# Kernel tuning notes

Hardware: AMD Instinct MI355X
Metric: run time of the kernel (lower is better)

Reference implementation:

```python
import jax, jax.numpy as jnp
import numpy as np

MAX_DISP = 192

def _conv(x, w, b=None, stride=1, pad=0):
    y = jax.lax.conv_general_dilated(x, w, (stride, stride), [(pad, pad), (pad, pad)],
                                     dimension_numbers=('NCHW', 'OIHW', 'NCHW'))
    return y if b is None else y + b[None, :, None, None]

def _inorm(x):  # InstanceNorm2d, affine=False
    m = x.mean((2, 3), keepdims=True)
    v = x.var((2, 3), keepdims=True)
    return (x - m) * jax.lax.rsqrt(v + 1e-5)

def _bnorm(x):  # BatchNorm2d at init (gamma=1, beta=0), batch stats
    m = x.mean((0, 2, 3), keepdims=True)
    v = x.var((0, 2, 3), keepdims=True)
    return (x - m) * jax.lax.rsqrt(v + 1e-5)

def _encoder(x, w1, b1, w2, b2, w3, b3, norm):
    # simplified BasicEncoder: two stride-2 convs -> 1/4 resolution, then 1x1 proj
    x = jax.nn.relu(norm(_conv(x, w1, b1, 2, 3)))
    x = jax.nn.relu(norm(_conv(x, w2, b2, 2, 1)))
    return _conv(x, w3, b3, 1, 0)

def _forward(image1, image2, fnet_w1, fnet_b1, fnet_w2, fnet_b2, fnet_w3, fnet_b3,
             cnet_w1, cnet_b1, cnet_w2, cnet_b2, cnet_w3, cnet_b3,
             bform_a, bform_b, bform_cd_w, bform_cd_b,
             gru_wz, gru_bz, gru_wr, gru_br, gru_wq, gru_bq,
             disp_w1, disp_b1, disp_w2, disp_b2):
    i1 = 2.0 * (image1 / 255.0) - 1.0
    i2 = 2.0 * (image2 / 255.0) - 1.0
    fmap1 = _encoder(i1, fnet_w1, fnet_b1, fnet_w2, fnet_b2, fnet_w3, fnet_b3, _inorm)
    fmap2 = _encoder(i2, fnet_w1, fnet_b1, fnet_w2, fnet_b2, fnet_w3, fnet_b3, _inorm)
    hidden = jnp.tanh(_encoder(i1, cnet_w1, cnet_b1, cnet_w2, cnet_b2, cnet_w3, cnet_b3, _bnorm))
    Wf = fmap1.shape[3]
    for d in range(MAX_DISP // 4):  # 48 sequential width-sweep steps, shrinking overlap
        f1 = fmap1[:, :, :, d:]
        f2 = fmap2[:, :, :, :Wf - d] if d > 0 else fmap2
        # BilinearForm: a(x) + b(y) + cd(x*y), all 1x1 convs
        feat = _conv(f1, bform_a) + _conv(f2, bform_b) + _conv(f1 * f2, bform_cd_w, bform_cd_b)
        h = hidden[:, :, :, d:]
        # gru_input = cat(h, feat); ConvGRU cats hidden again -> [h, h, feat] = 96 ch
        hx = jnp.concatenate([h, h, feat], axis=1)
        z = jax.nn.sigmoid(_conv(hx, gru_wz, gru_bz, 1, 1))
        r = jax.nn.sigmoid(_conv(hx, gru_wr, gru_br, 1, 1))
        q = jnp.tanh(_conv(jnp.concatenate([r * h, h, feat], axis=1), gru_wq, gru_bq, 1, 1))
        h = (1.0 - z) * h + z * q
        hidden = hidden.at[:, :, :, d:].set(h)  # in-place scatter back
    # DisparityHead: conv3x3 -> relu -> conv3x3, negated
    return -_conv(jax.nn.relu(_conv(hidden, disp_w1, disp_b1, 1, 1)), disp_w2, disp_b2, 1, 1)

def setup_inputs():
    key = jax.random.key(0)
    ks = jax.random.split(key, 16)
    B, H, W, D = 1, 384, 640, 32
    def n(k, shape, scale=0.05):
        return (jax.random.normal(k, shape) * scale).astype(jnp.float32)
    z = lambda c: jnp.zeros((c,), jnp.float32)
    return {
        'image1': jax.random.uniform(ks[0], (B, 3, H, W), jnp.float32) * 255.0,
        'image2': jax.random.uniform(ks[1], (B, 3, H, W), jnp.float32) * 255.0,
        'fnet_w1': n(ks[2], (D, 3, 7, 7)), 'fnet_b1': z(D),
        'fnet_w2': n(ks[3], (D, D, 3, 3)), 'fnet_b2': z(D),
        'fnet_w3': n(ks[4], (D, D, 1, 1)), 'fnet_b3': z(D),
        'cnet_w1': n(ks[5], (D, 3, 7, 7)), 'cnet_b1': z(D),
        'cnet_w2': n(ks[6], (D, D, 3, 3)), 'cnet_b2': z(D),
        'cnet_w3': n(ks[7], (D, D, 1, 1)), 'cnet_b3': z(D),
        'bform_a': n(ks[8], (D, D, 1, 1)), 'bform_b': n(ks[9], (D, D, 1, 1)),
        'bform_cd_w': n(ks[10], (D, D, 1, 1)), 'bform_cd_b': z(D),
        'gru_wz': n(ks[11], (D, 3 * D, 3, 3)), 'gru_bz': z(D),
        'gru_wr': n(ks[12], (D, 3 * D, 3, 3)), 'gru_br': z(D),
        'gru_wq': n(ks[13], (D, 3 * D, 3, 3)), 'gru_bq': z(D),
        'disp_w1': n(ks[14], (64, D, 3, 3)), 'disp_b1': z(64),
        'disp_w2': n(ks[15], (1, 64, 3, 3)), 'disp_b2': z(1),
    }

def reference(image1, image2, fnet_w1, fnet_b1, fnet_w2, fnet_b2, fnet_w3, fnet_b3,
              cnet_w1, cnet_b1, cnet_w2, cnet_b2, cnet_w3, cnet_b3,
              bform_a, bform_b, bform_cd_w, bform_cd_b,
              gru_wz, gru_bz, gru_wr, gru_br, gru_wq, gru_bq,
              disp_w1, disp_b1, disp_w2, disp_b2):
    return _forward(image1, image2, fnet_w1, fnet_b1, fnet_w2, fnet_b2, fnet_w3, fnet_b3,
                    cnet_w1, cnet_b1, cnet_w2, cnet_b2, cnet_w3, cnet_b3,
                    bform_a, bform_b, bform_cd_w, bform_cd_b,
                    gru_wz, gru_bz, gru_wr, gru_br, gru_wq, gru_bq,
                    disp_w1, disp_b1, disp_w2, disp_b2)
```

## Files before the change

kernel.cpp:

```cpp
#include <hip/hip_runtime.h>
#include <math.h>

#define H0 384
#define W0 640
#define H1 192
#define W1 320
#define H2 96
#define W2 160
#define NP1 (H1*W1)
#define NP2 (H2*W2)
#define ND  48
#define NBLK2 (NP2/256)
#define CHW ((size_t)32*NP2)
#define PW 162
#define PH 98
#define PSL (PH*PW)
#define PCHW ((size_t)32*PSL)

typedef float v2f __attribute__((ext_vector_type(2)));


__global__ void zero_buf_kernel(float* __restrict__ p, size_t n) {
    size_t i = (size_t)blockIdx.x*256 + threadIdx.x;
    size_t stride = (size_t)gridDim.x*256;
    for (; i < n; i += stride) p[i] = 0.f;
}

__device__ __forceinline__ void twr_dev(const float* __restrict__ in, float* __restrict__ out,
                                        int idx, int CI, int K, int CO) {
    int co = idx % CO;
    int t  = idx / CO;
    int k  = t % K;
    int ci = t / K;
    out[idx] = in[(co*CI + ci)*K + k];
}

__global__ void prep_all(const float* __restrict__ fnet_w1, const float* __restrict__ cnet_w1,
                         const float* __restrict__ fnet_w2, const float* __restrict__ cnet_w2,
                         const float* __restrict__ fnet_w3, const float* __restrict__ cnet_w3,
                         const float* __restrict__ bform_a, const float* __restrict__ bform_b,
                         const float* __restrict__ bform_cd_w, const float* __restrict__ disp_w1,
                         const float* __restrict__ gru_wz, const float* __restrict__ gru_wr,
                         const float* __restrict__ gru_wq,
                         float* __restrict__ we1f, float* __restrict__ we1c,
                         float* __restrict__ we2f, float* __restrict__ we2c,
                         float* __restrict__ w3f, float* __restrict__ w3c,
                         float* __restrict__ wat, float* __restrict__ wbt,
                         float* __restrict__ wct, float* __restrict__ wd1t,
                         float4* __restrict__ wzrpk, float2* __restrict__ wqpk,
                         float* __restrict__ stats) {
    int i = blockIdx.x*256 + threadIdx.x;
    if (i < 4704) { twr_dev(fnet_w1, we1f, i, 3, 49, 32); return; }
    i -= 4704;
    if (i < 4704) { twr_dev(cnet_w1, we1c, i, 3, 49, 32); return; }
    i -= 4704;
    if (i < 9216) { twr_dev(fnet_w2, we2f, i, 32, 9, 32); return; }
    i -= 9216;
    if (i < 9216) { twr_dev(cnet_w2, we2c, i, 32, 9, 32); return; }
    i -= 9216;
    if (i < 1024) { twr_dev(fnet_w3, w3f, i, 32, 1, 32); return; }
    i -= 1024;
    if (i < 1024) { twr_dev(cnet_w3, w3c, i, 32, 1, 32); return; }
    i -= 1024;
    if (i < 1024) { twr_dev(bform_a, wat, i, 32, 1, 32); return; }
    i -= 1024;
    if (i < 1024) { twr_dev(bform_b, wbt, i, 32, 1, 32); return; }
    i -= 1024;
    if (i < 1024) { twr_dev(bform_cd_w, wct, i, 32, 1, 32); return; }
    i -= 1024;
    if (i < 18432) { twr_dev(disp_w1, wd1t, i, 32, 9, 64); return; }
    i -= 18432;
    if (i < 9216) {
        int k  = i % 9;
        int ci = (i/9) % 64;
        int cg = i / (9*64);
        int co0 = cg*2, co1 = co0 + 1;
        float z0, z1, r0, r1;
        if (ci < 32) {
            z0 = gru_wz[(co0*96 + ci)*9 + k] + gru_wz[(co0*96 + ci + 32)*9 + k];
            z1 = gru_wz[(co1*96 + ci)*9 + k] + gru_wz[(co1*96 + ci + 32)*9 + k];
            r0 = gru_wr[(co0*96 + ci)*9 + k] + gru_wr[(co0*96 + ci + 32)*9 + k];
            r1 = gru_wr[(co1*96 + ci)*9 + k] + gru_wr[(co1*96 + ci + 32)*9 + k];
        } else {
            z0 = gru_wz[(co0*96 + ci + 32)*9 + k];
            z1 = gru_wz[(co1*96 + ci + 32)*9 + k];
            r0 = gru_wr[(co0*96 + ci + 32)*9 + k];
            r1 = gru_wr[(co1*96 + ci + 32)*9 + k];
        }
        wzrpk[i] = make_float4(z0, z1, r0, r1);
        return;
    }
    i -= 9216;
    if (i < 13824) {
        int k  = i % 9;
        int ci = (i/9) % 96;
        int cg = i / (9*96);
        wqpk[i] = make_float2(gru_wq[((cg*2)*96 + ci)*9 + k], gru_wq[((cg*2+1)*96 + ci)*9 + k]);
        return;
    }
    i -= 13824;
    if (i < 384) stats[i] = 0.f;
}

__global__ void pad_init_kernel(const float* __restrict__ hidden, float* __restrict__ hwork) {
    int idx = blockIdx.x*256 + threadIdx.x;
    if (idx >= 32*PSL) return;
    int c = idx / PSL;
    int r = idx % PSL;
    int py = r / PW, px = r % PW;
    int y = py - 1, x = px - 1;
    float v = 0.f;
    if ((unsigned)y < (unsigned)H2 && (unsigned)x < (unsigned)W2)
        v = hidden[c*NP2 + y*W2 + x];
    hwork[idx] = v;
}


__global__ __launch_bounds__(256, 4)
void conv7s2_dual(const float* __restrict__ img,
                  const float* __restrict__ wtf, const float* __restrict__ wtc,
                  const float* __restrict__ bf, const float* __restrict__ bc,
                  float* __restrict__ outf, float* __restrict__ outc) {
    int co8 = blockIdx.y*8;
    int sp = blockIdx.x*256 + threadIdx.x;
    int oy = sp / W1, ox = sp % W1;
    float af[8], ac[8];
    #pragma unroll
    for (int j = 0; j < 8; ++j) { af[j] = bf[co8+j]; ac[j] = bc[co8+j]; }
    for (int ci = 0; ci < 3; ++ci) {
        for (int ky = 0; ky < 7; ++ky) {
            int iy = 2*oy - 3 + ky;
            if ((unsigned)iy >= (unsigned)H0) continue;
            const float* row  = img + ci*(H0*W0) + iy*W0;
            int wbase = (ci*49 + ky*7)*32 + co8;
            #pragma unroll
            for (int kx = 0; kx < 7; ++kx) {
                int ix = 2*ox - 3 + kx;
                if ((unsigned)ix >= (unsigned)W0) continue;
                float v = row[ix]*(2.0f/255.0f) - 1.0f;
                const float4* wpf = (const float4*)(wtf + wbase + kx*32);
                const float4* wpc = (const float4*)(wtc + wbase + kx*32);
                float4 f0 = wpf[0], f1 = wpf[1];
                float4 c0 = wpc[0], c1 = wpc[1];
                af[0] += v*f0.x; af[1] += v*f0.y; af[2] += v*f0.z; af[3] += v*f0.w;
                af[4] += v*f1.x; af[5] += v*f1.y; af[6] += v*f1.z; af[7] += v*f1.w;
                ac[0] += v*c0.x; ac[1] += v*c0.y; ac[2] += v*c0.z; ac[3] += v*c0.w;
                ac[4] += v*c1.x; ac[5] += v*c1.y; ac[6] += v*c1.z; ac[7] += v*c1.w;
            }
        }
    }
    #pragma unroll
    for (int j = 0; j < 8; ++j) {
        outf[(co8+j)*NP1 + sp] = af[j];
        outc[(co8+j)*NP1 + sp] = ac[j];
    }
}

__global__ void conv7s2_v3(const float* __restrict__ img, const float* __restrict__ wt,
                           const float* __restrict__ b, float* __restrict__ out) {
    int cg = blockIdx.y;
    int co16 = cg*16;
    int sp = blockIdx.x*256 + threadIdx.x;
    int oy = sp / W1, ox = sp % W1;
    float acc[16];
    #pragma unroll
    for (int j = 0; j < 16; ++j) acc[j] = b[co16+j];
    for (int ci = 0; ci < 3; ++ci) {
        for (int ky = 0; ky < 7; ++ky) {
            int iy = 2*oy - 3 + ky;
            if ((unsigned)iy >= (unsigned)H0) continue;
            const float* row  = img + ci*(H0*W0) + iy*W0;
            const float* wrow = wt + (ci*49 + ky*7)*32 + co16;
            #pragma unroll
            for (int kx = 0; kx < 7; ++kx) {
                int ix = 2*ox - 3 + kx;
                if ((unsigned)ix >= (unsigned)W0) continue;
                float v = row[ix]*(2.0f/255.0f) - 1.0f;
                const float4* wp = (const float4*)(wrow + kx*32);
                #pragma unroll
                for (int j4 = 0; j4 < 4; ++j4) {
                    float4 w4 = wp[j4];
                    acc[4*j4+0] += v*w4.x; acc[4*j4+1] += v*w4.y;
                    acc[4*j4+2] += v*w4.z; acc[4*j4+3] += v*w4.w;
                }
            }
        }
    }
    #pragma unroll
    for (int j = 0; j < 16; ++j) out[(co16+j)*NP1 + sp] = acc[j];
}

__global__ void stats_partial_kernel(const float* __restrict__ x, int N, float* __restrict__ st) {
    int c = blockIdx.x >> 3, sl = blockIdx.x & 7;
    int chunk = N >> 3;
    const float4* p = (const float4*)(x + (size_t)c*N + (size_t)sl*chunk);
    int n4 = chunk >> 2;
    float s = 0.f, s2 = 0.f;
    for (int i = threadIdx.x; i < n4; i += 256) {
        float4 v = p[i];
        s  += v.x + v.y + v.z + v.w;
        s2 += v.x*v.x + v.y*v.y + v.z*v.z + v.w*v.w;
    }
    __shared__ float sh1[256], sh2[256];
    sh1[threadIdx.x] = s; sh2[threadIdx.x] = s2;
    __syncthreads();
    for (int o = 128; o > 0; o >>= 1) {
        if (threadIdx.x < o) { sh1[threadIdx.x] += sh1[threadIdx.x+o]; sh2[threadIdx.x] += sh2[threadIdx.x+o]; }
        __syncthreads();
    }
    if (threadIdx.x == 0) { atomicAdd(&st[2*c], sh1[0]); atomicAdd(&st[2*c+1], sh2[0]); }
}

__global__ void conv3s2_fused(const float* __restrict__ in, const float* __restrict__ st,
                              const float* __restrict__ wt, const float* __restrict__ b,
                              float* __restrict__ out) {
    int cg = blockIdx.x / NBLK2;
    int sp = (blockIdx.x % NBLK2)*256 + threadIdx.x;
    int co8 = cg*8;
    int oy = sp / W2, ox = sp % W2;
    float acc[8];
    #pragma unroll
    for (int j = 0; j < 8; ++j) acc[j] = b[co8+j];
    for (int ci = 0; ci < 32; ++ci) {
        float m    = st[2*ci] * (1.0f/NP1);
        float var  = st[2*ci+1] * (1.0f/NP1) - m*m;
        float rstd = rsqrtf(var + 1e-5f);
        const float* ip  = in + ci*NP1;
        const float* wci = wt + ci*9*32 + co8;
        #pragma unroll
        for (int ky = 0; ky < 3; ++ky) {
            int iy = 2*oy - 1 + ky;
            if ((unsigned)iy >= (unsigned)H1) continue;
            const float* row = ip + iy*W1;
            #pragma unroll
            for (int kx = 0; kx < 3; ++kx) {
                int ix = 2*ox - 1 + kx;
                if ((unsigned)ix >= (unsigned)W1) continue;
                float t = fmaxf((row[ix] - m)*rstd, 0.f);
                const float4* wp = (const float4*)(wci + (ky*3+kx)*32);
                float4 w0 = wp[0], w1 = wp[1];
                acc[0] += t*w0.x; acc[1] += t*w0.y; acc[2] += t*w0.z; acc[3] += t*w0.w;
                acc[4] += t*w1.x; acc[5] += t*w1.y; acc[6] += t*w1.z; acc[7] += t*w1.w;
            }
        }
    }
    #pragma unroll
    for (int j = 0; j < 8; ++j) out[(co8+j)*NP2 + sp] = acc[j];
}

__global__ void conv1x1_fused(const float* __restrict__ in, const float* __restrict__ st,
                              const float* __restrict__ wt, const float* __restrict__ b,
                              float* __restrict__ out, int mode) {
    int cg = blockIdx.x / NBLK2;
    int sp = (blockIdx.x % NBLK2)*256 + threadIdx.x;
    int co8 = cg*8;
    float acc[8];
    #pragma unroll
    for (int j = 0; j < 8; ++j) acc[j] = b[co8+j];
    for (int ci = 0; ci < 32; ++ci) {
        float m    = st[2*ci] * (1.0f/NP2);
        float var  = st[2*ci+1] * (1.0f/NP2) - m*m;
        float rstd = rsqrtf(var + 1e-5f);
        float t = fmaxf((in[ci*NP2 + sp] - m)*rstd, 0.f);
        const float4* wp = (const float4*)(wt + ci*32 + co8);
        float4 w0 = wp[0], w1 = wp[1];
        acc[0] += t*w0.x; acc[1] += t*w0.y; acc[2] += t*w0.z; acc[3] += t*w0.w;
        acc[4] += t*w1.x; acc[5] += t*w1.y; acc[6] += t*w1.z; acc[7] += t*w1.w;
    }
    #pragma unroll
    for (int j = 0; j < 8; ++j) {
        float a = acc[j];
        if (mode) a = tanhf(a);
        out[(co8+j)*NP2 + sp] = a;
    }
}


__global__ void feat0_pad_kernel(const float* __restrict__ fmap1, const float* __restrict__ fmap2,
                                 const float* __restrict__ wat, const float* __restrict__ wbt,
                                 const float* __restrict__ wct, const float* __restrict__ bc,
                                 float* __restrict__ featA) {
    int cg  = blockIdx.x / NBLK2;
    int sp  = (blockIdx.x % NBLK2)*256 + threadIdx.x;
    int y = sp / W2;
    int gx = sp % W2;
    int co8 = cg*8;
    float acc[8];
    #pragma unroll
    for (int j = 0; j < 8; ++j) acc[j] = bc[co8+j];
    for (int ci = 0; ci < 32; ++ci) {
        float f1 = fmap1[ci*NP2 + sp];
        float f2 = fmap2[ci*NP2 + sp];
        float f12 = f1*f2;
        const float4* ap = (const float4*)(wat + ci*32 + co8);
        const float4* bp = (const float4*)(wbt + ci*32 + co8);
        const float4* cp = (const float4*)(wct + ci*32 + co8);
        float4 a0 = ap[0], a1 = ap[1];
        float4 b0 = bp[0], b1 = bp[1];
        float4 c0 = cp[0], c1 = cp[1];
        acc[0] += f1*a0.x + f2*b0.x + f12*c0.x;
        acc[1] += f1*a0.y + f2*b0.y + f12*c0.y;
        acc[2] += f1*a0.z + f2*b0.z + f12*c0.z;
        acc[3] += f1*a0.w + f2*b0.w + f12*c0.w;
        acc[4] += f1*a1.x + f2*b1.x + f12*c1.x;
        acc[5] += f1*a1.y + f2*b1.y + f12*c1.y;
        acc[6] += f1*a1.z + f2*b1.z + f12*c1.z;
        acc[7] += f1*a1.w + f2*b1.w + f12*c1.w;
    }
    float* dst = featA + (size_t)(y+1)*PW + (gx+1);
    #pragma unroll
    for (int j = 0; j < 8; ++j) dst[(size_t)(co8+j)*PSL] = acc[j];
}


__global__ __launch_bounds__(256, 4)
void zrf_v6(const float* __restrict__ hworkA, const float* __restrict__ featA,
            const float* __restrict__ fmap1, const float* __restrict__ fmap2,
            const float4* __restrict__ wzrpk,
            const float* __restrict__ wat, const float* __restrict__ wbt,
            const float* __restrict__ wct, const float* __restrict__ bfc,
            const float* __restrict__ bz, const float* __restrict__ br,
            float* __restrict__ zbuf, float* __restrict__ rhpad,
            float* __restrict__ featB, int d, int Wd) {
    __shared__ v2f lwz[64*9], lwr[64*9];
    __shared__ v2f lfa[32], lfb[32], lfc[32];
    int cg  = blockIdx.y;
    int co0 = cg*2;
    {
        const float4* wsrc = wzrpk + (size_t)cg*576;
        for (int i = threadIdx.x; i < 576; i += 256) {
            float4 w = wsrc[i];
            lwz[i] = (v2f){w.x, w.y};
            lwr[i] = (v2f){w.z, w.w};
        }
        if (threadIdx.x < 32) {
            int ci = threadIdx.x;
            lfa[ci] = (v2f){wat[ci*32+co0], wat[ci*32+co0+1]};
            lfb[ci] = (v2f){wbt[ci*32+co0], wbt[ci*32+co0+1]};
            lfc[ci] = (v2f){wct[ci*32+co0], wct[ci*32+co0+1]};
        }
    }
    __syncthreads();
    int sp2 = blockIdx.x*256 + threadIdx.x;
    if (sp2 >= 48*Wd) return;
    int rp = sp2 / Wd;
    int lx = sp2 - rp*Wd;
    int y0 = rp*2;
    int gx = d + lx;
    size_t poff = (size_t)(y0+1)*PW + (gx+1);

    if (lx == 0) {
        #pragma unroll
        for (int j = 0; j < 2; ++j) {
            rhpad[(size_t)(co0+j)*PSL + poff - 1]      = 0.f;
            rhpad[(size_t)(co0+j)*PSL + poff + PW - 1] = 0.f;
        }
    }

    int dn = d + 1;
    if (dn < ND) {
        if (lx == 0) {
            #pragma unroll
            for (int j = 0; j < 2; ++j) {
                featB[(size_t)(co0+j)*PSL + poff]      = 0.f;
                featB[(size_t)(co0+j)*PSL + poff + PW] = 0.f;
            }
        } else {
            v2f f0 = (v2f){bfc[co0], bfc[co0+1]};
            v2f f1 = f0;
            int base1 = y0*W2 + gx;
            #pragma unroll 2
            for (int ci = 0; ci < 32; ++ci) {
                float a1 = fmap1[ci*NP2 + base1];
                float a2 = fmap1[ci*NP2 + base1 + W2];
                float b1 = fmap2[ci*NP2 + base1 - dn];
                float b2 = fmap2[ci*NP2 + base1 + W2 - dn];
                v2f wa = lfa[ci], wb = lfb[ci], wc = lfc[ci];
                f0 += wa*(v2f){a1,a1} + wb*(v2f){b1,b1} + wc*(v2f){a1*b1,a1*b1};
                f1 += wa*(v2f){a2,a2} + wb*(v2f){b2,b2} + wc*(v2f){a2*b2,a2*b2};
            }
            featB[(size_t)co0*PSL + poff]          = f0.x;
            featB[(size_t)(co0+1)*PSL + poff]      = f0.y;
            featB[(size_t)co0*PSL + poff + PW]     = f1.x;
            featB[(size_t)(co0+1)*PSL + poff + PW] = f1.y;
        }
    }

    v2f az0 = (v2f){bz[co0], bz[co0+1]}, az1 = az0;
    v2f ar0 = (v2f){br[co0], br[co0+1]}, ar1 = ar0;
    #pragma unroll
    for (int pass = 0; pass < 2; ++pass) {
        const float* p = (pass == 0 ? hworkA : featA) + poff;
        const v2f* wz = lwz + pass*288;
        const v2f* wr = lwr + pass*288;
        #pragma unroll 2
        for (int ci = 0; ci < 32; ++ci) {
            float v[12];
            #pragma unroll
            for (int r = 0; r < 4; ++r) {
                v[r*3+0] = p[(r-1)*PW - 1];
                v[r*3+1] = p[(r-1)*PW    ];
                v[r*3+2] = p[(r-1)*PW + 1];
            }
            #pragma unroll
            for (int k = 0; k < 9; ++k) {
                int ky = k/3, kx = k - 3*ky;
                float t0 = v[ky*3+kx];
                float t1 = v[(ky+1)*3+kx];
                v2f wzk = wz[k], wrk = wr[k];
                az0 += wzk*(v2f){t0,t0}; az1 += wzk*(v2f){t1,t1};
                ar0 += wrk*(v2f){t0,t0}; ar1 += wrk*(v2f){t1,t1};
            }
            p += PSL;
            wz += 9; wr += 9;
        }
    }
    v2f z0, z1, r0, r1;
    z0.x = 1.f/(1.f + __expf(-az0.x)); z0.y = 1.f/(1.f + __expf(-az0.y));
    z1.x = 1.f/(1.f + __expf(-az1.x)); z1.y = 1.f/(1.f + __expf(-az1.y));
    r0.x = 1.f/(1.f + __expf(-ar0.x)); r0.y = 1.f/(1.f + __expf(-ar0.y));
    r1.x = 1.f/(1.f + __expf(-ar1.x)); r1.y = 1.f/(1.f + __expf(-ar1.y));
    int ub = y0*W2 + gx;
    float h00 = hworkA[(size_t)co0*PSL + poff];
    float h01 = hworkA[(size_t)(co0+1)*PSL + poff];
    float h10 = hworkA[(size_t)co0*PSL + poff + PW];
    float h11 = hworkA[(size_t)(co0+1)*PSL + poff + PW];
    zbuf[(size_t)co0*NP2 + ub]          = z0.x;
    zbuf[(size_t)(co0+1)*NP2 + ub]      = z0.y;
    zbuf[(size_t)co0*NP2 + ub + W2]     = z1.x;
    zbuf[(size_t)(co0+1)*NP2 + ub + W2] = z1.y;
    rhpad[(size_t)co0*PSL + poff]          = r0.x*h00;
    rhpad[(size_t)(co0+1)*PSL + poff]      = r0.y*h01;
    rhpad[(size_t)co0*PSL + poff + PW]     = r1.x*h10;
    rhpad[(size_t)(co0+1)*PSL + poff + PW] = r1.y*h11;
}

__global__ __launch_bounds__(256, 4)
void qup_v6(const float* __restrict__ rhpad, const float* __restrict__ hworkA,
            const float* __restrict__ featA, const float* __restrict__ zbuf,
            const float2* __restrict__ qpk, const float* __restrict__ bq,
            float* __restrict__ hfinal, float* __restrict__ hworkB, int d, int Wd) {
    __shared__ v2f lw[96*9];
    int cg  = blockIdx.y;
    int co0 = cg*2;
    {
        const float2* wsrc = qpk + (size_t)cg*864;
        for (int i = threadIdx.x; i < 864; i += 256) {
            float2 w = wsrc[i];
            lw[i] = (v2f){w.x, w.y};
        }
    }
    __syncthreads();
    int sp2 = blockIdx.x*256 + threadIdx.x;
    if (sp2 >= 48*Wd) return;
    int rp = sp2 / Wd;
    int lx = sp2 - rp*Wd;
    int y0 = rp*2;
    int gx = d + lx;
    size_t poff = (size_t)(y0+1)*PW + (gx+1);

    v2f a0 = (v2f){bq[co0], bq[co0+1]};
    v2f a1 = a0;
    #pragma unroll
    for (int pass = 0; pass < 3; ++pass) {
        const float* p = (pass == 0 ? rhpad : (pass == 1 ? hworkA : featA)) + poff;
        const v2f* wp = lw + pass*288;
        #pragma unroll 2
        for (int ci = 0; ci < 32; ++ci) {
            float v[12];
            #pragma unroll
            for (int r = 0; r < 4; ++r) {
                v[r*3+0] = p[(r-1)*PW - 1];
                v[r*3+1] = p[(r-1)*PW    ];
                v[r*3+2] = p[(r-1)*PW + 1];
            }
            #pragma unroll
            for (int k = 0; k < 9; ++k) {
                int ky = k/3, kx = k - 3*ky;
                float t0 = v[ky*3+kx];
                float t1 = v[(ky+1)*3+kx];
                v2f wk = wp[k];
                a0 += wk*(v2f){t0,t0};
                a1 += wk*(v2f){t1,t1};
            }
            p += PSL;
            wp += 9;
        }
    }
    float q00 = tanhf(a0.x), q01 = tanhf(a0.y);
    float q10 = tanhf(a1.x), q11 = tanhf(a1.y);
    int ub = y0*W2 + gx;
    #pragma unroll
    for (int j = 0; j < 2; ++j) {
        float qa = (j == 0) ? q00 : q01;
        float qb = (j == 0) ? q10 : q11;
        size_t pidx = (size_t)(co0+j)*PSL + poff;
        size_t uidx = (size_t)(co0+j)*NP2 + ub;
        float z_a = zbuf[uidx];
        float z_b = zbuf[uidx + W2];
        float h_a = hworkA[pidx];
        float h_b = hworkA[pidx + PW];
        float hn_a = (1.f - z_a)*h_a + z_a*qa;
        float hn_b = (1.f - z_b)*h_b + z_b*qb;
        if (lx == 0 || d == ND-1) {
            hfinal[pidx]      = hn_a;
            hfinal[pidx + PW] = hn_b;
        }
        hworkB[pidx]      = (lx == 0) ? 0.f : hn_a;
        hworkB[pidx + PW] = (lx == 0) ? 0.f : hn_b;
    }
}


__global__ __launch_bounds__(256, 4)
void disp1_v6(const float* __restrict__ hfinal, const float* __restrict__ wt,
              const float* __restrict__ b, float* __restrict__ out) {
    __shared__ float4 lw[288];
    int cg  = blockIdx.y;
    int co0 = cg*4;
    for (int i = threadIdx.x; i < 288; i += 256)
        lw[i] = *(const float4*)&wt[i*64 + co0];
    __syncthreads();
    int sp2 = blockIdx.x*256 + threadIdx.x;
    int y0 = (sp2 / W2)*2;
    int gx = sp2 % W2;
    size_t poff = (size_t)(y0+1)*PW + (gx+1);
    float4 bb = *(const float4*)&b[co0];
    float acc0[4] = {bb.x, bb.y, bb.z, bb.w};
    float acc1[4] = {bb.x, bb.y, bb.z, bb.w};
    const float* p = hfinal + poff;
    #pragma unroll 2
    for (int ci = 0; ci < 32; ++ci) {
        float v[12];
        #pragma unroll
        for (int r = 0; r < 4; ++r) {
            v[r*3+0] = p[(r-1)*PW - 1];
            v[r*3+1] = p[(r-1)*PW    ];
            v[r*3+2] = p[(r-1)*PW + 1];
        }
        #pragma unroll
        for (int k = 0; k < 9; ++k) {
            int ky = k/3, kx = k - 3*ky;
            float t0 = v[ky*3+kx];
            float t1 = v[(ky+1)*3+kx];
            float4 w = lw[ci*9+k];
            acc0[0] += t0*w.x; acc0[1] += t0*w.y; acc0[2] += t0*w.z; acc0[3] += t0*w.w;
            acc1[0] += t1*w.x; acc1[1] += t1*w.y; acc1[2] += t1*w.z; acc1[3] += t1*w.w;
        }
        p += PSL;
    }
    int ub = y0*W2 + gx;
    #pragma unroll
    for (int j = 0; j < 4; ++j) {
        out[(co0+j)*NP2 + ub]      = fmaxf(acc0[j], 0.f);
        out[(co0+j)*NP2 + ub + W2] = fmaxf(acc1[j], 0.f);
    }
}

__global__ void disp2_part_kernel(const float* __restrict__ in, const float* __restrict__ w,
                                  float* __restrict__ part) {
    __shared__ float lw[8*9];
    int g  = blockIdx.x / NBLK2;
    int sp = (blockIdx.x % NBLK2)*256 + threadIdx.x;
    if (threadIdx.x < 72) lw[threadIdx.x] = w[g*72 + threadIdx.x];
    __syncthreads();
    int y = sp / W2, x = sp % W2;
    float acc = 0.f;
    #pragma unroll
    for (int ci = 0; ci < 8; ++ci) {
        const float* ip = in + (g*8 + ci)*NP2;
        #pragma unroll
        for (int dy = 0; dy < 3; ++dy) {
            int ys = y+dy-1; if ((unsigned)ys >= (unsigned)H2) continue;
            const float* row = ip + ys*W2;
            #pragma unroll
            for (int dx = 0; dx < 3; ++dx) {
                int xs = x+dx-1; if ((unsigned)xs >= (unsigned)W2) continue;
                acc += lw[ci*9+dy*3+dx] * row[xs];
            }
        }
    }
    part[g*NP2 + sp] = acc;
}

__global__ void disp2_comb_kernel(const float* __restrict__ part, const float* __restrict__ b,
                                  float* __restrict__ out) {
    int sp = blockIdx.x*256 + threadIdx.x;
    float acc = b[0];
    #pragma unroll
    for (int g = 0; g < 8; ++g) acc += part[g*NP2 + sp];
    out[sp] = -acc;
}


extern "C" void kernel_launch(void* const* d_in, const int* in_sizes, int n_in,
                              void* d_out, int out_size, void* d_ws, size_t ws_size,
                              hipStream_t stream) {
    const float* image1   = (const float*)d_in[0];
    const float* image2   = (const float*)d_in[1];
    const float* fnet_w1  = (const float*)d_in[2];
    const float* fnet_b1  = (const float*)d_in[3];
    const float* fnet_w2  = (const float*)d_in[4];
    const float* fnet_b2  = (const float*)d_in[5];
    const float* fnet_w3  = (const float*)d_in[6];
    const float* fnet_b3  = (const float*)d_in[7];
    const float* cnet_w1  = (const float*)d_in[8];
    const float* cnet_b1  = (const float*)d_in[9];
    const float* cnet_w2  = (const float*)d_in[10];
    const float* cnet_b2  = (const float*)d_in[11];
    const float* cnet_w3  = (const float*)d_in[12];
    const float* cnet_b3  = (const float*)d_in[13];
    const float* bform_a  = (const float*)d_in[14];
    const float* bform_b  = (const float*)d_in[15];
    const float* bform_cd_w = (const float*)d_in[16];
    const float* bform_cd_b = (const float*)d_in[17];
    const float* gru_wz   = (const float*)d_in[18];
    const float* gru_bz   = (const float*)d_in[19];
    const float* gru_wr   = (const float*)d_in[20];
    const float* gru_br   = (const float*)d_in[21];
    const float* gru_wq   = (const float*)d_in[22];
    const float* gru_bq   = (const float*)d_in[23];
    const float* disp_w1  = (const float*)d_in[24];
    const float* disp_b1  = (const float*)d_in[25];
    const float* disp_w2  = (const float*)d_in[26];
    const float* disp_b2  = (const float*)d_in[27];

    float* ws = (float*)d_ws;
    size_t o = 0;
    float* e1f    = ws + o; o += (size_t)32*NP1;
    float* e1c    = ws + o; o += (size_t)32*NP1;
    float* e2     = ws + o; o += CHW;
    float* fmap1  = ws + o; o += CHW;
    float* fmap2  = ws + o; o += CHW;
    float* hidden = ws + o; o += CHW;
    float* zbuf   = ws + o; o += CHW;
    float* hwork0 = ws + o; o += PCHW;
    float* hwork1 = ws + o; o += PCHW;
    float* rhpad  = ws + o; o += PCHW;
    float* feat0  = ws + o; o += PCHW;
    float* feat1  = ws + o; o += PCHW;
    float* hfinal = ws + o; o += PCHW;
    float* stats  = ws + o; o += 384;
    float* wzrpk  = ws + o; o += 16*64*9*4;
    float* wqpk   = ws + o; o += 16*96*9*2;
    float* we1f   = ws + o; o += 3*49*32;
    float* we1c   = ws + o; o += 3*49*32;
    float* we2f   = ws + o; o += 32*9*32;
    float* we2c   = ws + o; o += 32*9*32;
    float* w3f    = ws + o; o += 32*32;
    float* w3c    = ws + o; o += 32*32;
    float* wat    = ws + o; o += 32*32;
    float* wbt    = ws + o; o += 32*32;
    float* wct    = ws + o; o += 32*32;
    float* wd1t   = ws + o; o += 32*9*64;
    float* disp1buf  = e1f;
    float* disp2part = e1c;

    prep_all<<<(74816 + 255)/256, 256, 0, stream>>>(
        fnet_w1, cnet_w1, fnet_w2, cnet_w2, fnet_w3, cnet_w3,
        bform_a, bform_b, bform_cd_w, disp_w1, gru_wz, gru_wr, gru_wq,
        we1f, we1c, we2f, we2c, w3f, w3c, wat, wbt, wct, wd1t,
        (float4*)wzrpk, (float2*)wqpk, stats);

    conv7s2_dual<<<dim3(NP1/256, 4), 256, 0, stream>>>(image1, we1f, we1c, fnet_b1, cnet_b1,
                                                       e1f, e1c);
    stats_partial_kernel<<<256, 256, 0, stream>>>(e1f, NP1, stats+0);
    stats_partial_kernel<<<256, 256, 0, stream>>>(e1c, NP1, stats+64);
    conv3s2_fused<<<4*NBLK2, 256, 0, stream>>>(e1f, stats+0, we2f, fnet_b2, e2);
    stats_partial_kernel<<<256, 256, 0, stream>>>(e2, NP2, stats+128);
    conv1x1_fused<<<4*NBLK2, 256, 0, stream>>>(e2, stats+128, w3f, fnet_b3, fmap1, 0);
    conv3s2_fused<<<4*NBLK2, 256, 0, stream>>>(e1c, stats+64, we2c, cnet_b2, e2);
    stats_partial_kernel<<<256, 256, 0, stream>>>(e2, NP2, stats+192);
    conv1x1_fused<<<4*NBLK2, 256, 0, stream>>>(e2, stats+192, w3c, cnet_b3, hidden, 1);
    conv7s2_v3<<<dim3(NP1/256, 2), 256, 0, stream>>>(image2, we1f, fnet_b1, e1f);
    stats_partial_kernel<<<256, 256, 0, stream>>>(e1f, NP1, stats+256);
    conv3s2_fused<<<4*NBLK2, 256, 0, stream>>>(e1f, stats+256, we2f, fnet_b2, e2);
    stats_partial_kernel<<<256, 256, 0, stream>>>(e2, NP2, stats+320);
    conv1x1_fused<<<4*NBLK2, 256, 0, stream>>>(e2, stats+320, w3f, fnet_b3, fmap2, 0);

    zero_buf_kernel<<<2048, 256, 0, stream>>>(hwork1, 5*PCHW);
    pad_init_kernel<<<(32*PSL+255)/256, 256, 0, stream>>>(hidden, hwork0);
    feat0_pad_kernel<<<4*NBLK2, 256, 0, stream>>>(fmap1, fmap2, wat, wbt, wct,
                                                  bform_cd_b, feat0);

    float* hwA = hwork0; float* hwB = hwork1;
    float* ftA = feat0;  float* ftB = feat1;
    for (int d = 0; d < ND; ++d) {
        int Wd = W2 - d;
        int nblk = (48*Wd + 255)/256;
        zrf_v6<<<dim3(nblk, 16), 256, 0, stream>>>(hwA, ftA, fmap1, fmap2,
                                                   (const float4*)wzrpk,
                                                   wat, wbt, wct, bform_cd_b,
                                                   gru_bz, gru_br, zbuf, rhpad, ftB, d, Wd);
        qup_v6<<<dim3(nblk, 16), 256, 0, stream>>>(rhpad, hwA, ftA, zbuf,
                                                   (const float2*)wqpk, gru_bq,
                                                   hfinal, hwB, d, Wd);
        float* t;
        t = hwA; hwA = hwB; hwB = t;
        t = ftA; ftA = ftB; ftB = t;
    }

    disp1_v6<<<dim3(30, 16), 256, 0, stream>>>(hfinal, wd1t, disp_b1, disp1buf);
    disp2_part_kernel<<<8*NBLK2, 256, 0, stream>>>(disp1buf, disp_w2, disp2part);
    disp2_comb_kernel<<<NBLK2, 256, 0, stream>>>(disp2part, disp_b2, (float*)d_out);
}
```

Measured before the change: 2.965 ms.

## Split q-gate conv: compute h/feat part alongside z/r gates, finish r*h part after

The first kernel now launches twice as many blocks. Half compute the z and r gates; the other half compute the next bilinear feature map plus the partial q-gate convolution over the hidden and feat inputs, written to a new qpart buffer. The second kernel then convolves only the r*h input and adds qpart before tanh. This moves two thirds of the q-gate work off the serial dependency on r, balancing work across the two launches and raising parallelism in the first one. The cost is an extra global buffer written and read each step, plus duplicated reads of hidden and feat.

```diff
diff --git a/kernel.cpp b/kernel.cpp
--- a/kernel.cpp
+++ b/kernel.cpp
@@ -314,24 +314,32 @@
 
 
 __global__ __launch_bounds__(256, 4)
-void zrf_v6(const float* __restrict__ hworkA, const float* __restrict__ featA,
-            const float* __restrict__ fmap1, const float* __restrict__ fmap2,
-            const float4* __restrict__ wzrpk,
-            const float* __restrict__ wat, const float* __restrict__ wbt,
-            const float* __restrict__ wct, const float* __restrict__ bfc,
-            const float* __restrict__ bz, const float* __restrict__ br,
-            float* __restrict__ zbuf, float* __restrict__ rhpad,
-            float* __restrict__ featB, int d, int Wd) {
-    __shared__ v2f lwz[64*9], lwr[64*9];
+void zrq_a(const float* __restrict__ hworkA, const float* __restrict__ featA,
+           const float* __restrict__ fmap1, const float* __restrict__ fmap2,
+           const float4* __restrict__ wzrpk, const float2* __restrict__ wqpk,
+           const float* __restrict__ wat, const float* __restrict__ wbt,
+           const float* __restrict__ wct, const float* __restrict__ bfc,
+           const float* __restrict__ bz, const float* __restrict__ br,
+           float* __restrict__ zbuf, float* __restrict__ rhpad,
+           float* __restrict__ featB, float* __restrict__ qpart,
+           int d, int Wd) {
+    __shared__ v2f lws[1152];
     __shared__ v2f lfa[32], lfb[32], lfc[32];
-    int cg  = blockIdx.y;
+    int cg  = blockIdx.y >> 1;
+    int job = blockIdx.y & 1;
     int co0 = cg*2;
-    {
+    if (job == 0) {
         const float4* wsrc = wzrpk + (size_t)cg*576;
         for (int i = threadIdx.x; i < 576; i += 256) {
             float4 w = wsrc[i];
-            lwz[i] = (v2f){w.x, w.y};
-            lwr[i] = (v2f){w.z, w.w};
+            lws[i]       = (v2f){w.x, w.y};
+            lws[576 + i] = (v2f){w.z, w.w};
+        }
+    } else {
+        const float2* wsrc = wqpk + (size_t)cg*864 + 288;
+        for (int i = threadIdx.x; i < 576; i += 256) {
+            float2 w = wsrc[i];
+            lws[i] = (v2f){w.x, w.y};
         }
         if (threadIdx.x < 32) {
             int ci = threadIdx.x;
@@ -348,51 +356,156 @@
     int y0 = rp*2;
     int gx = d + lx;
     size_t poff = (size_t)(y0+1)*PW + (gx+1);
-
-    if (lx == 0) {
-        #pragma unroll
-        for (int j = 0; j < 2; ++j) {
-            rhpad[(size_t)(co0+j)*PSL + poff - 1]      = 0.f;
-            rhpad[(size_t)(co0+j)*PSL + poff + PW - 1] = 0.f;
-        }
-    }
-
-    int dn = d + 1;
-    if (dn < ND) {
+    int ub = y0*W2 + gx;
+
+    if (job == 0) {
         if (lx == 0) {
             #pragma unroll
             for (int j = 0; j < 2; ++j) {
-                featB[(size_t)(co0+j)*PSL + poff]      = 0.f;
-                featB[(size_t)(co0+j)*PSL + poff + PW] = 0.f;
-            }
-        } else {
-            v2f f0 = (v2f){bfc[co0], bfc[co0+1]};
-            v2f f1 = f0;
-            int base1 = y0*W2 + gx;
+                rhpad[(size_t)(co0+j)*PSL + poff - 1]      = 0.f;
+                rhpad[(size_t)(co0+j)*PSL + poff + PW - 1] = 0.f;
+            }
+        }
+        v2f az0 = (v2f){bz[co0], bz[co0+1]}, az1 = az0;
+        v2f ar0 = (v2f){br[co0], br[co0+1]}, ar1 = ar0;
+        #pragma unroll
+        for (int pass = 0; pass < 2; ++pass) {
+            const float* p = (pass == 0 ? hworkA : featA) + poff;
+            const v2f* wz = lws + pass*288;
+            const v2f* wr = lws + 576 + pass*288;
             #pragma unroll 2
             for (int ci = 0; ci < 32; ++ci) {
-                float a1 = fmap1[ci*NP2 + base1];
-                float a2 = fmap1[ci*NP2 + base1 + W2];
-                float b1 = fmap2[ci*NP2 + base1 - dn];
-                float b2 = fmap2[ci*NP2 + base1 + W2 - dn];
-                v2f wa = lfa[ci], wb = lfb[ci], wc = lfc[ci];
-                f0 += wa*(v2f){a1,a1} + wb*(v2f){b1,b1} + wc*(v2f){a1*b1,a1*b1};
-                f1 += wa*(v2f){a2,a2} + wb*(v2f){b2,b2} + wc*(v2f){a2*b2,a2*b2};
-            }
-            featB[(size_t)co0*PSL + poff]          = f0.x;
-            featB[(size_t)(co0+1)*PSL + poff]      = f0.y;
-            featB[(size_t)co0*PSL + poff + PW]     = f1.x;
-            featB[(size_t)(co0+1)*PSL + poff + PW] = f1.y;
-        }
-    }
-
-    v2f az0 = (v2f){bz[co0], bz[co0+1]}, az1 = az0;
-    v2f ar0 = (v2f){br[co0], br[co0+1]}, ar1 = ar0;
-    #pragma unroll
-    for (int pass = 0; pass < 2; ++pass) {
-        const float* p = (pass == 0 ? hworkA : featA) + poff;
-        const v2f* wz = lwz + pass*288;
-        const v2f* wr = lwr + pass*288;
+                float v[12];
+                #pragma unroll
+                for (int r = 0; r < 4; ++r) {
+                    v[r*3+0] = p[(r-1)*PW - 1];
+                    v[r*3+1] = p[(r-1)*PW    ];
+                    v[r*3+2] = p[(r-1)*PW + 1];
+                }
+                #pragma unroll
+                for (int k = 0; k < 9; ++k) {
+                    int ky = k/3, kx = k - 3*ky;
+                    float t0 = v[ky*3+kx];
+                    float t1 = v[(ky+1)*3+kx];
+                    v2f wzk = wz[k], wrk = wr[k];
+                    az0 += wzk*(v2f){t0,t0}; az1 += wzk*(v2f){t1,t1};
+                    ar0 += wrk*(v2f){t0,t0}; ar1 += wrk*(v2f){t1,t1};
+                }
+                p += PSL;
+                wz += 9; wr += 9;
+            }
+        }
+        v2f z0, z1, r0, r1;
+        z0.x = 1.f/(1.f + __expf(-az0.x)); z0.y = 1.f/(1.f + __expf(-az0.y));
+        z1.x = 1.f/(1.f + __expf(-az1.x)); z1.y = 1.f/(1.f + __expf(-az1.y));
+        r0.x = 1.f/(1.f + __expf(-ar0.x)); r0.y = 1.f/(1.f + __expf(-ar0.y));
+        r1.x = 1.f/(1.f + __expf(-ar1.x)); r1.y = 1.f/(1.f + __expf(-ar1.y));
+        float h00 = hworkA[(size_t)co0*PSL + poff];
+        float h01 = hworkA[(size_t)(co0+1)*PSL + poff];
+        float h10 = hworkA[(size_t)co0*PSL + poff + PW];
+        float h11 = hworkA[(size_t)(co0+1)*PSL + poff + PW];
+        zbuf[(size_t)co0*NP2 + ub]          = z0.x;
+        zbuf[(size_t)(co0+1)*NP2 + ub]      = z0.y;
+        zbuf[(size_t)co0*NP2 + ub + W2]     = z1.x;
+        zbuf[(size_t)(co0+1)*NP2 + ub + W2] = z1.y;
+        rhpad[(size_t)co0*PSL + poff]          = r0.x*h00;
+        rhpad[(size_t)(co0+1)*PSL + poff]      = r0.y*h01;
+        rhpad[(size_t)co0*PSL + poff + PW]     = r1.x*h10;
+        rhpad[(size_t)(co0+1)*PSL + poff + PW] = r1.y*h11;
+    } else {
+        int dn = d + 1;
+        if (dn < ND) {
+            if (lx == 0) {
+                #pragma unroll
+                for (int j = 0; j < 2; ++j) {
+                    featB[(size_t)(co0+j)*PSL + poff]      = 0.f;
+                    featB[(size_t)(co0+j)*PSL + poff + PW] = 0.f;
+                }
+            } else {
+                v2f f0 = (v2f){bfc[co0], bfc[co0+1]};
+                v2f f1 = f0;
+                int base1 = y0*W2 + gx;
+                #pragma unroll 2
+                for (int ci = 0; ci < 32; ++ci) {
+                    float a1 = fmap1[ci*NP2 + base1];
+                    float a2 = fmap1[ci*NP2 + base1 + W2];
+                    float b1 = fmap2[ci*NP2 + base1 - dn];
+                    float b2 = fmap2[ci*NP2 + base1 + W2 - dn];
+                    v2f wa = lfa[ci], wb = lfb[ci], wc = lfc[ci];
+                    f0 += wa*(v2f){a1,a1} + wb*(v2f){b1,b1} + wc*(v2f){a1*b1,a1*b1};
+                    f1 += wa*(v2f){a2,a2} + wb*(v2f){b2,b2} + wc*(v2f){a2*b2,a2*b2};
+                }
+                featB[(size_t)co0*PSL + poff]          = f0.x;
+                featB[(size_t)(co0+1)*PSL + poff]      = f0.y;
+                featB[(size_t)co0*PSL + poff + PW]     = f1.x;
+                featB[(size_t)(co0+1)*PSL + poff + PW] = f1.y;
+            }
+        }
+        v2f a0 = (v2f){0.f, 0.f};
+        v2f a1 = a0;
+        #pragma unroll
+        for (int pass = 0; pass < 2; ++pass) {
+            const float* p = (pass == 0 ? hworkA : featA) + poff;
+            const v2f* wp = lws + pass*288;
+            #pragma unroll 2
+            for (int ci = 0; ci < 32; ++ci) {
+                float v[12];
+                #pragma unroll
+                for (int r = 0; r < 4; ++r) {
+                    v[r*3+0] = p[(r-1)*PW - 1];
+                    v[r*3+1] = p[(r-1)*PW    ];
+                    v[r*3+2] = p[(r-1)*PW + 1];
+                }
+                #pragma unroll
+                for (int k = 0; k < 9; ++k) {
+                    int ky = k/3, kx = k - 3*ky;
+                    float t0 = v[ky*3+kx];
+                    float t1 = v[(ky+1)*3+kx];
+                    v2f wk = wp[k];
+                    a0 += wk*(v2f){t0,t0};
+                    a1 += wk*(v2f){t1,t1};
+                }
+                p += PSL;
+                wp += 9;
+            }
+        }
+        qpart[(size_t)co0*NP2 + ub]          = a0.x;
+        qpart[(size_t)(co0+1)*NP2 + ub]      = a0.y;
+        qpart[(size_t)co0*NP2 + ub + W2]     = a1.x;
+        qpart[(size_t)(co0+1)*NP2 + ub + W2] = a1.y;
+    }
+}
+
+__global__ __launch_bounds__(256, 4)
+void q_fin(const float* __restrict__ rhpad, const float* __restrict__ hworkA,
+           const float* __restrict__ zbuf, const float* __restrict__ qpart,
+           const float2* __restrict__ wqpk, const float* __restrict__ bq,
+           float* __restrict__ hfinal, float* __restrict__ hworkB, int d, int Wd) {
+    __shared__ v2f lw[288];
+    int cg  = blockIdx.y;
+    int co0 = cg*2;
+    {
+        const float2* wsrc = wqpk + (size_t)cg*864;
+        for (int i = threadIdx.x; i < 288; i += 256) {
+            float2 w = wsrc[i];
+            lw[i] = (v2f){w.x, w.y};
+        }
+    }
+    __syncthreads();
+    int sp2 = blockIdx.x*256 + threadIdx.x;
+    if (sp2 >= 48*Wd) return;
+    int rp = sp2 / Wd;
+    int lx = sp2 - rp*Wd;
+    int y0 = rp*2;
+    int gx = d + lx;
+    size_t poff = (size_t)(y0+1)*PW + (gx+1);
+    int ub = y0*W2 + gx;
+
+    v2f a0 = (v2f){bq[co0], bq[co0+1]};
+    v2f a1 = a0;
+    {
+        const float* p = rhpad + poff;
+        const v2f* wp = lw;
         #pragma unroll 2
         for (int ci = 0; ci < 32; ++ci) {
             float v[12];
@@ -407,78 +520,6 @@
                 int ky = k/3, kx = k - 3*ky;
                 float t0 = v[ky*3+kx];
                 float t1 = v[(ky+1)*3+kx];
-                v2f wzk = wz[k], wrk = wr[k];
-                az0 += wzk*(v2f){t0,t0}; az1 += wzk*(v2f){t1,t1};
-                ar0 += wrk*(v2f){t0,t0}; ar1 += wrk*(v2f){t1,t1};
-            }
-            p += PSL;
-            wz += 9; wr += 9;
-        }
-    }
-    v2f z0, z1, r0, r1;
-    z0.x = 1.f/(1.f + __expf(-az0.x)); z0.y = 1.f/(1.f + __expf(-az0.y));
-    z1.x = 1.f/(1.f + __expf(-az1.x)); z1.y = 1.f/(1.f + __expf(-az1.y));
-    r0.x = 1.f/(1.f + __expf(-ar0.x)); r0.y = 1.f/(1.f + __expf(-ar0.y));
-    r1.x = 1.f/(1.f + __expf(-ar1.x)); r1.y = 1.f/(1.f + __expf(-ar1.y));
-    int ub = y0*W2 + gx;
-    float h00 = hworkA[(size_t)co0*PSL + poff];
-    float h01 = hworkA[(size_t)(co0+1)*PSL + poff];
-    float h10 = hworkA[(size_t)co0*PSL + poff + PW];
-    float h11 = hworkA[(size_t)(co0+1)*PSL + poff + PW];
-    zbuf[(size_t)co0*NP2 + ub]          = z0.x;
-    zbuf[(size_t)(co0+1)*NP2 + ub]      = z0.y;
-    zbuf[(size_t)co0*NP2 + ub + W2]     = z1.x;
-    zbuf[(size_t)(co0+1)*NP2 + ub + W2] = z1.y;
-    rhpad[(size_t)co0*PSL + poff]          = r0.x*h00;
-    rhpad[(size_t)(co0+1)*PSL + poff]      = r0.y*h01;
-    rhpad[(size_t)co0*PSL + poff + PW]     = r1.x*h10;
-    rhpad[(size_t)(co0+1)*PSL + poff + PW] = r1.y*h11;
-}
-
-__global__ __launch_bounds__(256, 4)
-void qup_v6(const float* __restrict__ rhpad, const float* __restrict__ hworkA,
-            const float* __restrict__ featA, const float* __restrict__ zbuf,
-            const float2* __restrict__ qpk, const float* __restrict__ bq,
-            float* __restrict__ hfinal, float* __restrict__ hworkB, int d, int Wd) {
-    __shared__ v2f lw[96*9];
-    int cg  = blockIdx.y;
-    int co0 = cg*2;
-    {
-        const float2* wsrc = qpk + (size_t)cg*864;
-        for (int i = threadIdx.x; i < 864; i += 256) {
-            float2 w = wsrc[i];
-            lw[i] = (v2f){w.x, w.y};
-        }
-    }
-    __syncthreads();
-    int sp2 = blockIdx.x*256 + threadIdx.x;
-    if (sp2 >= 48*Wd) return;
-    int rp = sp2 / Wd;
-    int lx = sp2 - rp*Wd;
-    int y0 = rp*2;
-    int gx = d + lx;
-    size_t poff = (size_t)(y0+1)*PW + (gx+1);
-
-    v2f a0 = (v2f){bq[co0], bq[co0+1]};
-    v2f a1 = a0;
-    #pragma unroll
-    for (int pass = 0; pass < 3; ++pass) {
-        const float* p = (pass == 0 ? rhpad : (pass == 1 ? hworkA : featA)) + poff;
-        const v2f* wp = lw + pass*288;
-        #pragma unroll 2
-        for (int ci = 0; ci < 32; ++ci) {
-            float v[12];
-            #pragma unroll
-            for (int r = 0; r < 4; ++r) {
-                v[r*3+0] = p[(r-1)*PW - 1];
-                v[r*3+1] = p[(r-1)*PW    ];
-                v[r*3+2] = p[(r-1)*PW + 1];
-            }
-            #pragma unroll
-            for (int k = 0; k < 9; ++k) {
-                int ky = k/3, kx = k - 3*ky;
-                float t0 = v[ky*3+kx];
-                float t1 = v[(ky+1)*3+kx];
                 v2f wk = wp[k];
                 a0 += wk*(v2f){t0,t0};
                 a1 += wk*(v2f){t1,t1};
@@ -487,9 +528,12 @@
             wp += 9;
         }
     }
+    a0.x += qpart[(size_t)co0*NP2 + ub];
+    a0.y += qpart[(size_t)(co0+1)*NP2 + ub];
+    a1.x += qpart[(size_t)co0*NP2 + ub + W2];
+    a1.y += qpart[(size_t)(co0+1)*NP2 + ub + W2];
     float q00 = tanhf(a0.x), q01 = tanhf(a0.y);
     float q10 = tanhf(a1.x), q11 = tanhf(a1.y);
-    int ub = y0*W2 + gx;
     #pragma unroll
     for (int j = 0; j < 2; ++j) {
         float qa = (j == 0) ? q00 : q01;
@@ -634,6 +678,7 @@
     float* fmap2  = ws + o; o += CHW;
     float* hidden = ws + o; o += CHW;
     float* zbuf   = ws + o; o += CHW;
+    float* qpart  = ws + o; o += CHW;
     float* hwork0 = ws + o; o += PCHW;
     float* hwork1 = ws + o; o += PCHW;
     float* rhpad  = ws + o; o += PCHW;
@@ -688,13 +733,14 @@
     for (int d = 0; d < ND; ++d) {
         int Wd = W2 - d;
         int nblk = (48*Wd + 255)/256;
-        zrf_v6<<<dim3(nblk, 16), 256, 0, stream>>>(hwA, ftA, fmap1, fmap2,
-                                                   (const float4*)wzrpk,
-                                                   wat, wbt, wct, bform_cd_b,
-                                                   gru_bz, gru_br, zbuf, rhpad, ftB, d, Wd);
-        qup_v6<<<dim3(nblk, 16), 256, 0, stream>>>(rhpad, hwA, ftA, zbuf,
-                                                   (const float2*)wqpk, gru_bq,
-                                                   hfinal, hwB, d, Wd);
+        zrq_a<<<dim3(nblk, 32), 256, 0, stream>>>(hwA, ftA, fmap1, fmap2,
+                                                  (const float4*)wzrpk, (const float2*)wqpk,
+                                                  wat, wbt, wct, bform_cd_b,
+                                                  gru_bz, gru_br, zbuf, rhpad, ftB, qpart,
+                                                  d, Wd);
+        q_fin<<<dim3(nblk, 16), 256, 0, stream>>>(rhpad, hwA, zbuf, qpart,
+                                                  (const float2*)wqpk, gru_bq,
+                                                  hfinal, hwB, d, Wd);
         float* t;
         t = hwA; hwA = hwB; hwB = t;
         t = ftA; ftA = ftB; ftB = t;
```

Result: faster. 2.681 ms (median of 2 runs) (-9.6%).
